# Optimization experiments

Hardware: AMD Instinct MI355X
Metric: run time of the kernel (lower is better)

## Reference

```python
import jax, jax.numpy as jnp
import numpy as np

N_NODES = 100000
N_EDGES = 1000000
D = 64
N_GRAPHS = 128
N_LAYERS = 3
BN_EPS = 1e-5


def setup_inputs() -> dict:
    key = jax.random.key(0)
    ks = jax.random.split(key, 8)
    x = jax.random.normal(ks[0], (N_NODES, D), dtype=jnp.float32)
    edge_index = jax.random.randint(ks[1], (2, N_EDGES), 0, N_NODES, dtype=jnp.int64)
    edge_attr = jax.random.uniform(ks[2], (N_EDGES,), dtype=jnp.float32)
    batch = jnp.sort(jax.random.randint(ks[3], (N_NODES,), 0, N_GRAPHS, dtype=jnp.int64))
    # xavier-uniform linear weights [L, out, in], zero conv bias (PyG GCNConv adds bias after aggregation)
    limit = float(np.sqrt(6.0 / (D + D)))
    W = jax.random.uniform(ks[4], (N_LAYERS, D, D), minval=-limit, maxval=limit, dtype=jnp.float32)
    b = jnp.zeros((N_LAYERS, D), dtype=jnp.float32)
    prelu_a = jnp.asarray(0.25, dtype=jnp.float32)  # single PReLU shared across layers
    bn_w = jnp.ones((N_LAYERS, D), dtype=jnp.float32)
    bn_b = jnp.zeros((N_LAYERS, D), dtype=jnp.float32)
    return {"x": x, "edge_index": edge_index, "edge_attr": edge_attr, "batch": batch,
            "W": W, "b": b, "prelu_a": prelu_a, "bn_w": bn_w, "bn_b": bn_b}


def reference(x, edge_index, edge_attr, batch, W, b, prelu_a, bn_w, bn_b):
    src, dst = edge_index[0], edge_index[1]
    h = x
    pooled = []
    for i in range(N_LAYERS):
        # GCNConv (normalize=False, add_self_loops=False): lin -> weighted scatter-add -> bias
        h = h @ W[i].T                                      # [N, D]
        msg = h[src] * edge_attr[:, None]                   # [E, D] gather + scale
        h = jax.ops.segment_sum(msg, dst, num_segments=N_NODES) + b[i]
        # shared PReLU
        h = jnp.where(h >= 0, h, prelu_a * h)
        # BatchNorm1d (training mode: biased batch stats over nodes)
        mean = jnp.mean(h, axis=0)
        var = jnp.mean((h - mean) ** 2, axis=0)
        h = (h - mean) * jax.lax.rsqrt(var + BN_EPS) * bn_w[i] + bn_b[i]
        pooled.append(jax.ops.segment_sum(h, batch, num_segments=N_GRAPHS))
    global_rep = jnp.concatenate(pooled, axis=1)            # [G, L*D]
    x_stack = pooled[-1]                                    # [G, D]
    return (global_rep, x_stack)
```

## Files before the change

kernel.cpp:

```cpp
#include <hip/hip_runtime.h>

#define NNODES 100000
#define NEDGES 1000000
#define DIM 64
#define NGRAPHS 128
#define NLAYERS 3
#define BN_EPS 1e-5f

#define BINSZ 8
#define NBINS 12500
#define GBLK 256
#define ECHUNK 3907
#define SLICES 4

#define OFF_EDGES   0
#define OFF_BINBASE 2000000
#define OFF_AGG     2012544
#define OFF_YBF     8412544
#define OFF_XBF     11612544
#define OFF_CNT     14812544
#define OFF_OFS     16412544
#define OFF_BTOT    18012544
#define OFF_GSUM4   18025088
#define OFF_PQ4     18057856
#define OFF_SCALE   18090624
#define OFF_SHIFT   18090816
#define OFF_END     18091008

__device__ __forceinline__ unsigned pack_bf16(float a, float b) {
    unsigned ua = __float_as_uint(a), ub = __float_as_uint(b);
    ua = (ua + 0x7FFFu + ((ua >> 16) & 1u)) >> 16;
    ub = (ub + 0x7FFFu + ((ub >> 16) & 1u)) & 0xFFFF0000u;
    return ua | ub;
}

__global__ __launch_bounds__(1024) void count_kernel(const int* __restrict__ ei,
                                                     const float* __restrict__ x,
                                                     const int* __restrict__ batch,
                                                     unsigned short* __restrict__ counts,
                                                     unsigned* __restrict__ xbf,
                                                     int* __restrict__ endv) {
    __shared__ int hist[NBINS];
    const int tid = threadIdx.x, blk = blockIdx.x;
    for (int i = tid; i < NBINS; i += 1024) hist[i] = 0;
    __syncthreads();
    const int e0 = blk * ECHUNK, e1 = min(NEDGES, e0 + ECHUNK);
    for (int e = e0 + tid; e < e1; e += 1024)
        atomicAdd(&hist[ei[NEDGES + e] >> 3], 1);
    __syncthreads();
    unsigned short* crow = counts + (size_t)blk * NBINS;
    for (int bin = tid; bin < NBINS; bin += 1024)
        crow[bin] = (unsigned short)hist[bin];
    const int gtid = blk * 1024 + tid;
    for (int i = gtid; i < NNODES * 32; i += GBLK * 1024) {
        const float2 v = *(const float2*)(x + (size_t)i * 2);
        xbf[i] = pack_bf16(v.x, v.y);
    }
    for (int i = gtid; i < NNODES; i += GBLK * 1024) {
        const int b0 = batch[i];
        const int b1 = (i + 1 < NNODES) ? batch[i + 1] : NGRAPHS;
        for (int g = b0; g < b1; ++g) endv[g] = i + 1;
        if (i == 0)
            for (int g = 0; g < b0; ++g) endv[g] = 0;
    }
}

__global__ __launch_bounds__(256) void s1_kernel(const unsigned short* __restrict__ counts,
                                                 unsigned short* __restrict__ offs,
                                                 int* __restrict__ btot) {
    const int bin = blockIdx.x * 256 + threadIdx.x;
    if (bin >= NBINS) return;
    int run = 0;
    for (int blk = 0; blk < GBLK; ++blk) {
        const int v = counts[(size_t)blk * NBINS + bin];
        offs[(size_t)blk * NBINS + bin] = (unsigned short)run;
        run += v;
    }
    btot[bin] = run;
}

__global__ __launch_bounds__(1024) void s2_kernel(const int* __restrict__ btot,
                                                  int* __restrict__ binBase) {
    __shared__ int wsum[16];
    const int t = threadIdx.x, wid = t >> 6, lane = t & 63;
    int running = 0;
    for (int b = 0; b < NBINS; b += 1024) {
        const int i = b + t;
        const int v = (i < NBINS) ? btot[i] : 0;
        int s = v;
        for (int off = 1; off < 64; off <<= 1) {
            int x = __shfl_up(s, off);
            if (lane >= off) s += x;
        }
        __syncthreads();
        if (lane == 63) wsum[wid] = s;
        __syncthreads();
        int pw = 0, tot = 0;
#pragma unroll
        for (int k = 0; k < 16; ++k) {
            const int x = wsum[k];
            tot += x;
            if (k < wid) pw += x;
        }
        if (i < NBINS) binBase[i] = running + pw + s - v;
        running += tot;
    }
    if (t == 0) binBase[NBINS] = running;
}

__global__ __launch_bounds__(1024) void scatter_kernel(const int* __restrict__ ei,
                                                       const float* __restrict__ ea,
                                                       const int* __restrict__ binBase,
                                                       const unsigned short* __restrict__ offs,
                                                       int2* __restrict__ edges) {
    __shared__ int cur[NBINS];
    const int tid = threadIdx.x, blk = blockIdx.x;
    const unsigned short* orow = offs + (size_t)blk * NBINS;
    for (int i = tid; i < NBINS; i += 1024)
        cur[i] = binBase[i] + (int)orow[i];
    __syncthreads();
    const int e0 = blk * ECHUNK, e1 = min(NEDGES, e0 + ECHUNK);
    for (int e = e0 + tid; e < e1; e += 1024) {
        const int dst = ei[NEDGES + e];
        const int src = ei[e];
        const float w = ea[e];
        const int pos = atomicAdd(&cur[dst >> 3], 1);
        edges[pos] = make_int2((src << 3) | (dst & (BINSZ - 1)), __float_as_int(w));
    }
}

template <bool FIRST>
__global__ __launch_bounds__(256) void agg_kernel(const unsigned* __restrict__ hbf,
                                                  const float* __restrict__ scale,
                                                  const float* __restrict__ shift,
                                                  const int* __restrict__ binBase,
                                                  const int2* __restrict__ edges,
                                                  float* __restrict__ agg) {
    __shared__ float accAll[4][2][BINSZ * 64];
    const int w = threadIdx.x >> 6, lane = threadIdx.x & 63;
    const int bin = blockIdx.x * 4 + w;
    const int half = lane >> 5, p = lane & 31, c0 = 2 * p;
    float* ac = accAll[w][half];
#pragma unroll
    for (int r = 0; r < BINSZ; ++r) *(float2*)&ac[r * 64 + c0] = make_float2(0.f, 0.f);
    float sc0 = 1.f, sc1 = 1.f, sh0 = 0.f, sh1 = 0.f;
    if (!FIRST) { sc0 = scale[c0]; sc1 = scale[c0 + 1]; sh0 = shift[c0]; sh1 = shift[c0 + 1]; }
    const int beg = binBase[bin], end = binBase[bin + 1];
    for (int j = beg; j < end; j += 64) {
        const int n = min(64, end - j);
        int2 ed = (j + lane < end) ? edges[j + lane] : make_int2(0, 0);
        const int n16 = n & ~15;
        int t = 0;
        for (; t < n16; t += 16) {
            int sd_[8]; float wt_[8]; unsigned u_[8];
#pragma unroll
            for (int q = 0; q < 8; ++q) {
                const int ii = t + 2 * q + half;
                sd_[q] = __shfl(ed.x, ii);
                wt_[q] = __int_as_float(__shfl(ed.y, ii));
            }
#pragma unroll
            for (int q = 0; q < 8; ++q) u_[q] = hbf[(size_t)(sd_[q] >> 3) * 32 + p];
#pragma unroll
            for (int q = 0; q < 8; ++q) {
                float h0 = __uint_as_float(u_[q] << 16);
                float h1 = __uint_as_float(u_[q] & 0xFFFF0000u);
                if (!FIRST) { h0 = fmaf(h0, sc0, sh0); h1 = fmaf(h1, sc1, sh1); }
                float2* a2 = (float2*)&ac[(sd_[q] & 7) * 64 + c0];
                float2 v = *a2;
                v.x = fmaf(wt_[q], h0, v.x);
                v.y = fmaf(wt_[q], h1, v.y);
                *a2 = v;
            }
        }
        for (; t < n; t += 2) {
            const int ii = min(t + half, n - 1);
            const int sd = __shfl(ed.x, ii);
            float wt = __int_as_float(__shfl(ed.y, ii));
            if (t + half >= n) wt = 0.f;
            const unsigned u = hbf[(size_t)(sd >> 3) * 32 + p];
            float h0 = __uint_as_float(u << 16);
            float h1 = __uint_as_float(u & 0xFFFF0000u);
            if (!FIRST) { h0 = fmaf(h0, sc0, sh0); h1 = fmaf(h1, sc1, sh1); }
            float2* a2 = (float2*)&ac[(sd & 7) * 64 + c0];
            float2 v = *a2;
            v.x = fmaf(wt, h0, v.x);
            v.y = fmaf(wt, h1, v.y);
            *a2 = v;
        }
    }
    const int nodeBase = bin * BINSZ;
#pragma unroll
    for (int r = 0; r < BINSZ; ++r)
        agg[(size_t)(nodeBase + r) * 64 + lane] =
            accAll[w][0][r * 64 + lane] + accAll[w][1][r * 64 + lane];
}

__global__ __launch_bounds__(256) void gemm_kernel(const float* __restrict__ agg,
                                                   const float* __restrict__ W,
                                                   const float* __restrict__ bias,
                                                   const float* __restrict__ pa_ptr,
                                                   unsigned* __restrict__ ybf) {
    __shared__ float As[128 * 68];
    __shared__ float Wt[64 * 68];
    const int tid = threadIdx.x;
    const int base = blockIdx.x * 128;
    for (int i = tid; i < 2048; i += 256) {
        const int r = i >> 4;
        const int q = (i & 15) * 4;
        const int row = base + r;
        float4 v = make_float4(0.f, 0.f, 0.f, 0.f);
        if (row < NNODES) v = *(const float4*)(agg + (size_t)row * 64 + q);
        *(float4*)&As[r * 68 + q] = v;
    }
    for (int i = tid; i < 4096; i += 256)
        Wt[(i & 63) * 68 + (i >> 6)] = W[i];
    __syncthreads();

    const int tc = tid & 7;
    const int tr = tid >> 3;
    float acc[4][8];
#pragma unroll
    for (int j = 0; j < 4; ++j)
#pragma unroll
        for (int c = 0; c < 8; ++c) acc[j][c] = 0.f;

    for (int kc = 0; kc < 16; ++kc) {
        const int k0 = kc * 4;
        float Af[4][4];
#pragma unroll
        for (int j = 0; j < 4; ++j) {
            const float4 t = *(const float4*)&As[(tr + 32 * j) * 68 + k0];
            Af[j][0] = t.x; Af[j][1] = t.y; Af[j][2] = t.z; Af[j][3] = t.w;
        }
#pragma unroll
        for (int kk = 0; kk < 4; ++kk) {
            const float4 w0 = *(const float4*)&Wt[(k0 + kk) * 68 + tc * 8];
            const float4 w1 = *(const float4*)&Wt[(k0 + kk) * 68 + tc * 8 + 4];
#pragma unroll
            for (int j = 0; j < 4; ++j) {
                const float a = Af[j][kk];
                acc[j][0] = fmaf(a, w0.x, acc[j][0]);
                acc[j][1] = fmaf(a, w0.y, acc[j][1]);
                acc[j][2] = fmaf(a, w0.z, acc[j][2]);
                acc[j][3] = fmaf(a, w0.w, acc[j][3]);
                acc[j][4] = fmaf(a, w1.x, acc[j][4]);
                acc[j][5] = fmaf(a, w1.y, acc[j][5]);
                acc[j][6] = fmaf(a, w1.z, acc[j][6]);
                acc[j][7] = fmaf(a, w1.w, acc[j][7]);
            }
        }
    }

    const float pa = *pa_ptr;
    const float4 b0 = *(const float4*)(bias + tc * 8);
    const float4 b1 = *(const float4*)(bias + tc * 8 + 4);
#pragma unroll
    for (int j = 0; j < 4; ++j) {
        const int row = base + tr + 32 * j;
        if (row >= NNODES) continue;
        float o[8];
        o[0] = acc[j][0] + b0.x; o[1] = acc[j][1] + b0.y;
        o[2] = acc[j][2] + b0.z; o[3] = acc[j][3] + b0.w;
        o[4] = acc[j][4] + b1.x; o[5] = acc[j][5] + b1.y;
        o[6] = acc[j][6] + b1.z; o[7] = acc[j][7] + b1.w;
#pragma unroll
        for (int c = 0; c < 8; ++c) o[c] = (o[c] >= 0.f) ? o[c] : pa * o[c];
        uint4 pk;
        pk.x = pack_bf16(o[0], o[1]);
        pk.y = pack_bf16(o[2], o[3]);
        pk.z = pack_bf16(o[4], o[5]);
        pk.w = pack_bf16(o[6], o[7]);
        *(uint4*)(ybf + (size_t)row * 32 + tc * 4) = pk;
    }
}

__global__ __launch_bounds__(256) void stats_kernel(const unsigned* __restrict__ ybf,
                                                    const int* __restrict__ endv,
                                                    float* __restrict__ gsum4,
                                                    float* __restrict__ pQ4) {
    __shared__ float red[2][32][66];
    const int g = blockIdx.x >> 2, s = blockIdx.x & 3;
    const int t = threadIdx.x, rg = t >> 3, cg = t & 7;
    const int g0 = (g == 0) ? 0 : endv[g - 1];
    const int g1 = endv[g];
    const int len = g1 - g0;
    const int q0 = g0 + (len * s) / SLICES;
    const int q1 = g0 + (len * (s + 1)) / SLICES;
    float sm[8], sq[8];
#pragma unroll
    for (int k = 0; k < 8; ++k) { sm[k] = 0.f; sq[k] = 0.f; }
    for (int r = q0 + rg; r < q1; r += 32) {
        const uint4 u4 = *(const uint4*)&ybf[(size_t)r * 32 + cg * 4];
        const unsigned uu[4] = {u4.x, u4.y, u4.z, u4.w};
#pragma unroll
        for (int k = 0; k < 4; ++k) {
            const float f0 = __uint_as_float(uu[k] << 16);
            const float f1 = __uint_as_float(uu[k] & 0xFFFF0000u);
            sm[2 * k] += f0; sm[2 * k + 1] += f1;
            sq[2 * k] = fmaf(f0, f0, sq[2 * k]);
            sq[2 * k + 1] = fmaf(f1, f1, sq[2 * k + 1]);
        }
    }
#pragma unroll
    for (int k = 0; k < 8; ++k) {
        red[0][rg][cg * 8 + k] = sm[k];
        red[1][rg][cg * 8 + k] = sq[k];
    }
    __syncthreads();
    if (t < 128) {
        const int which = t >> 6, c = t & 63;
        float a = 0.f;
#pragma unroll
        for (int k = 0; k < 32; ++k) a += red[which][k][c];
        if (which == 0) gsum4[blockIdx.x * 64 + c] = a;
        else            pQ4[blockIdx.x * 64 + c] = a;
    }
}

__global__ __launch_bounds__(512) void finalize_kernel(const float* __restrict__ gsum4,
                                                       const float* __restrict__ pQ4,
                                                       const int* __restrict__ endv,
                                                       const float* __restrict__ bn_w,
                                                       const float* __restrict__ bn_b,
                                                       float* __restrict__ scale,
                                                       float* __restrict__ shift,
                                                       float* __restrict__ out, int layer) {
    __shared__ float rS[8][64], rQ[8][64];
    __shared__ float ssc[64], ssh[64];
    const int tid = threadIdx.x;
    const int c = tid & 63, pp = tid >> 6;
    float S = 0.f, Q = 0.f;
    for (int sl = pp; sl < NGRAPHS * SLICES; sl += 8) {
        S += gsum4[sl * 64 + c];
        Q += pQ4[sl * 64 + c];
    }
    rS[pp][c] = S; rQ[pp][c] = Q;
    __syncthreads();
    if (tid < 64) {
        float SS = 0.f, QQ = 0.f;
#pragma unroll
        for (int k = 0; k < 8; ++k) { SS += rS[k][c]; QQ += rQ[k][c]; }
        const float mean = SS * (1.f / NNODES);
        const float var = fmaxf(QQ * (1.f / NNODES) - mean * mean, 0.f);
        const float inv = rsqrtf(var + BN_EPS);
        const float scv = inv * bn_w[c];
        const float shv = bn_b[c] - mean * scv;
        ssc[c] = scv; ssh[c] = shv;
        scale[c] = scv; shift[c] = shv;
    }
    __syncthreads();
    for (int idx = tid; idx < NGRAPHS * 64; idx += 512) {
        const int g = idx >> 6, ch = idx & 63;
        float gs = 0.f;
#pragma unroll
        for (int sl = 0; sl < SLICES; ++sl) gs += gsum4[(g * SLICES + sl) * 64 + ch];
        const int cnt = endv[g] - ((g == 0) ? 0 : endv[g - 1]);
        const float pooled = gs * ssc[ch] + (float)cnt * ssh[ch];
        out[g * (NLAYERS * 64) + layer * 64 + ch] = pooled;
        if (layer == NLAYERS - 1) out[NGRAPHS * NLAYERS * 64 + idx] = pooled;
    }
}

extern "C" void kernel_launch(void* const* d_in, const int* in_sizes, int n_in,
                              void* d_out, int out_size, void* d_ws, size_t ws_size,
                              hipStream_t stream) {
    const float* x     = (const float*)d_in[0];
    const int*   ei    = (const int*)d_in[1];
    const float* ea    = (const float*)d_in[2];
    const int*   batch = (const int*)d_in[3];
    const float* W     = (const float*)d_in[4];
    const float* b     = (const float*)d_in[5];
    const float* pa    = (const float*)d_in[6];
    const float* bn_w  = (const float*)d_in[7];
    const float* bn_b  = (const float*)d_in[8];
    float* out = (float*)d_out;
    float* ws  = (float*)d_ws;
    int*   wsi = (int*)d_ws;

    int2*           edges   = (int2*)(wsi + OFF_EDGES);
    int*            binBase = wsi + OFF_BINBASE;
    float*          agg     = ws + OFF_AGG;
    unsigned*       ybf     = (unsigned*)(wsi + OFF_YBF);
    unsigned*       xbf     = (unsigned*)(wsi + OFF_XBF);
    unsigned short* counts  = (unsigned short*)(wsi + OFF_CNT);
    unsigned short* offs    = (unsigned short*)(wsi + OFF_OFS);
    int*            btot    = wsi + OFF_BTOT;
    float*          gsum4   = ws + OFF_GSUM4;
    float*          pQ4     = ws + OFF_PQ4;
    float*          scaleA  = ws + OFF_SCALE;
    float*          shiftA  = ws + OFF_SHIFT;
    int*            endv    = wsi + OFF_END;

    count_kernel<<<GBLK, 1024, 0, stream>>>(ei, x, batch, counts, xbf, endv);
    s1_kernel<<<(NBINS + 255) / 256, 256, 0, stream>>>(counts, offs, btot);
    s2_kernel<<<1, 1024, 0, stream>>>(btot, binBase);
    scatter_kernel<<<GBLK, 1024, 0, stream>>>(ei, ea, binBase, offs, edges);

    for (int l = 0; l < NLAYERS; ++l) {
        if (l == 0)
            agg_kernel<true><<<NBINS / 4, 256, 0, stream>>>(xbf, nullptr, nullptr,
                                                            binBase, edges, agg);
        else
            agg_kernel<false><<<NBINS / 4, 256, 0, stream>>>(ybf, scaleA + (l - 1) * 64,
                                                             shiftA + (l - 1) * 64,
                                                             binBase, edges, agg);
        gemm_kernel<<<(NNODES + 127) / 128, 256, 0, stream>>>(agg, W + l * 4096, b + l * 64,
                                                              pa, ybf);
        stats_kernel<<<NGRAPHS * SLICES, 256, 0, stream>>>(ybf, endv, gsum4, pQ4);
        finalize_kernel<<<1, 512, 0, stream>>>(gsum4, pQ4, endv, bn_w + l * 64,
                                               bn_b + l * 64, scaleA + l * 64,
                                               shiftA + l * 64, out, l);
    }
}
```

Measured before the change: 295.3 us.

## Store aggregation output as bf16 and fuse BN finalize into stats via last-block counter

The aggregation kernel now writes its per-node sums as packed bf16 instead of fp32, and the GEMM unpacks them. This halves the traffic of the agg intermediate. Separately, the stats and finalize kernels are merged: the last block to finish, found through an atomic counter with threadfences, computes the BN scale and shift and the pooled outputs, which removes one launch per layer. The cost is an extra bf16 rounding of the aggregated values before the GEMM, and the counters must be reset, which count_kernel does.

```diff
diff --git a/kernel.cpp b/kernel.cpp
--- a/kernel.cpp
+++ b/kernel.cpp
@@ -12,6 +12,7 @@
 #define GBLK 256
 #define ECHUNK 3907
 #define SLICES 4
+#define SBLK (NGRAPHS * SLICES)
 
 #define OFF_EDGES   0
 #define OFF_BINBASE 2000000
@@ -26,6 +27,7 @@
 #define OFF_SCALE   18090624
 #define OFF_SHIFT   18090816
 #define OFF_END     18091008
+#define OFF_CTR     18091136
 
 __device__ __forceinline__ unsigned pack_bf16(float a, float b) {
     unsigned ua = __float_as_uint(a), ub = __float_as_uint(b);
@@ -33,13 +35,16 @@
     ub = (ub + 0x7FFFu + ((ub >> 16) & 1u)) & 0xFFFF0000u;
     return ua | ub;
 }
+__device__ __forceinline__ float bflo(unsigned u) { return __uint_as_float(u << 16); }
+__device__ __forceinline__ float bfhi(unsigned u) { return __uint_as_float(u & 0xFFFF0000u); }
 
 __global__ __launch_bounds__(1024) void count_kernel(const int* __restrict__ ei,
                                                      const float* __restrict__ x,
                                                      const int* __restrict__ batch,
                                                      unsigned short* __restrict__ counts,
                                                      unsigned* __restrict__ xbf,
-                                                     int* __restrict__ endv) {
+                                                     int* __restrict__ endv,
+                                                     int* __restrict__ ctr) {
     __shared__ int hist[NBINS];
     const int tid = threadIdx.x, blk = blockIdx.x;
     for (int i = tid; i < NBINS; i += 1024) hist[i] = 0;
@@ -63,6 +68,7 @@
         if (i == 0)
             for (int g = 0; g < b0; ++g) endv[g] = 0;
     }
+    if (gtid < NLAYERS) ctr[gtid] = 0;
 }
 
 __global__ __launch_bounds__(256) void s1_kernel(const unsigned short* __restrict__ counts,
@@ -135,7 +141,7 @@
                                                   const float* __restrict__ shift,
                                                   const int* __restrict__ binBase,
                                                   const int2* __restrict__ edges,
-                                                  float* __restrict__ agg) {
+                                                  unsigned* __restrict__ aggbf) {
     __shared__ float accAll[4][2][BINSZ * 64];
     const int w = threadIdx.x >> 6, lane = threadIdx.x & 63;
     const int bin = blockIdx.x * 4 + w;
@@ -163,8 +169,8 @@
             for (int q = 0; q < 8; ++q) u_[q] = hbf[(size_t)(sd_[q] >> 3) * 32 + p];
 #pragma unroll
             for (int q = 0; q < 8; ++q) {
-                float h0 = __uint_as_float(u_[q] << 16);
-                float h1 = __uint_as_float(u_[q] & 0xFFFF0000u);
+                float h0 = bflo(u_[q]);
+                float h1 = bfhi(u_[q]);
                 if (!FIRST) { h0 = fmaf(h0, sc0, sh0); h1 = fmaf(h1, sc1, sh1); }
                 float2* a2 = (float2*)&ac[(sd_[q] & 7) * 64 + c0];
                 float2 v = *a2;
@@ -179,8 +185,8 @@
             float wt = __int_as_float(__shfl(ed.y, ii));
             if (t + half >= n) wt = 0.f;
             const unsigned u = hbf[(size_t)(sd >> 3) * 32 + p];
-            float h0 = __uint_as_float(u << 16);
-            float h1 = __uint_as_float(u & 0xFFFF0000u);
+            float h0 = bflo(u);
+            float h1 = bfhi(u);
             if (!FIRST) { h0 = fmaf(h0, sc0, sh0); h1 = fmaf(h1, sc1, sh1); }
             float2* a2 = (float2*)&ac[(sd & 7) * 64 + c0];
             float2 v = *a2;
@@ -191,12 +197,16 @@
     }
     const int nodeBase = bin * BINSZ;
 #pragma unroll
-    for (int r = 0; r < BINSZ; ++r)
-        agg[(size_t)(nodeBase + r) * 64 + lane] =
-            accAll[w][0][r * 64 + lane] + accAll[w][1][r * 64 + lane];
-}
-
-__global__ __launch_bounds__(256) void gemm_kernel(const float* __restrict__ agg,
+    for (int i = 0; i < 4; ++i) {
+        const int idx = lane + 64 * i;
+        const int r = idx >> 5, p2 = idx & 31;
+        const float2 a0 = *(const float2*)&accAll[w][0][r * 64 + 2 * p2];
+        const float2 a1 = *(const float2*)&accAll[w][1][r * 64 + 2 * p2];
+        aggbf[(size_t)(nodeBase + r) * 32 + p2] = pack_bf16(a0.x + a1.x, a0.y + a1.y);
+    }
+}
+
+__global__ __launch_bounds__(256) void gemm_kernel(const unsigned* __restrict__ aggbf,
                                                    const float* __restrict__ W,
                                                    const float* __restrict__ bias,
                                                    const float* __restrict__ pa_ptr,
@@ -207,11 +217,14 @@
     const int base = blockIdx.x * 128;
     for (int i = tid; i < 2048; i += 256) {
         const int r = i >> 4;
-        const int q = (i & 15) * 4;
+        const int q = i & 15;
         const int row = base + r;
         float4 v = make_float4(0.f, 0.f, 0.f, 0.f);
-        if (row < NNODES) v = *(const float4*)(agg + (size_t)row * 64 + q);
-        *(float4*)&As[r * 68 + q] = v;
+        if (row < NNODES) {
+            const uint2 u = *(const uint2*)&aggbf[(size_t)row * 32 + q * 2];
+            v = make_float4(bflo(u.x), bfhi(u.x), bflo(u.y), bfhi(u.y));
+        }
+        *(float4*)&As[r * 68 + q * 4] = v;
     }
     for (int i = tid; i < 4096; i += 256)
         Wt[(i & 63) * 68 + (i >> 6)] = W[i];
@@ -275,13 +288,20 @@
     }
 }
 
-__global__ __launch_bounds__(256) void stats_kernel(const unsigned* __restrict__ ybf,
-                                                    const int* __restrict__ endv,
-                                                    float* __restrict__ gsum4,
-                                                    float* __restrict__ pQ4) {
+__global__ __launch_bounds__(256) void statsfin_kernel(const unsigned* __restrict__ ybf,
+                                                       const int* __restrict__ endv,
+                                                       float* __restrict__ gsum4,
+                                                       float* __restrict__ pQ4,
+                                                       const float* __restrict__ bn_w,
+                                                       const float* __restrict__ bn_b,
+                                                       float* __restrict__ scale,
+                                                       float* __restrict__ shift,
+                                                       float* __restrict__ out, int layer,
+                                                       int* __restrict__ ctr) {
     __shared__ float red[2][32][66];
+    __shared__ int amLast;
     const int g = blockIdx.x >> 2, s = blockIdx.x & 3;
-    const int t = threadIdx.x, rg = t >> 3, cg = t & 7;
+    const int tid = threadIdx.x, rg = tid >> 3, cg = tid & 7;
     const int g0 = (g == 0) ? 0 : endv[g - 1];
     const int g1 = endv[g];
     const int len = g1 - g0;
@@ -295,8 +315,8 @@
         const unsigned uu[4] = {u4.x, u4.y, u4.z, u4.w};
 #pragma unroll
         for (int k = 0; k < 4; ++k) {
-            const float f0 = __uint_as_float(uu[k] << 16);
-            const float f1 = __uint_as_float(uu[k] & 0xFFFF0000u);
+            const float f0 = bflo(uu[k]);
+            const float f1 = bfhi(uu[k]);
             sm[2 * k] += f0; sm[2 * k + 1] += f1;
             sq[2 * k] = fmaf(f0, f0, sq[2 * k]);
             sq[2 * k + 1] = fmaf(f1, f1, sq[2 * k + 1]);
@@ -308,30 +328,27 @@
         red[1][rg][cg * 8 + k] = sq[k];
     }
     __syncthreads();
-    if (t < 128) {
-        const int which = t >> 6, c = t & 63;
+    if (tid < 128) {
+        const int which = tid >> 6, c = tid & 63;
         float a = 0.f;
 #pragma unroll
         for (int k = 0; k < 32; ++k) a += red[which][k][c];
         if (which == 0) gsum4[blockIdx.x * 64 + c] = a;
         else            pQ4[blockIdx.x * 64 + c] = a;
     }
-}
-
-__global__ __launch_bounds__(512) void finalize_kernel(const float* __restrict__ gsum4,
-                                                       const float* __restrict__ pQ4,
-                                                       const int* __restrict__ endv,
-                                                       const float* __restrict__ bn_w,
-                                                       const float* __restrict__ bn_b,
-                                                       float* __restrict__ scale,
-                                                       float* __restrict__ shift,
-                                                       float* __restrict__ out, int layer) {
-    __shared__ float rS[8][64], rQ[8][64];
+    __syncthreads();
+    if (tid == 0) {
+        __threadfence();
+        amLast = (atomicAdd(ctr, 1) == SBLK - 1);
+    }
+    __syncthreads();
+    if (!amLast) return;
+    __threadfence();
+    __shared__ float rS[4][64], rQ[4][64];
     __shared__ float ssc[64], ssh[64];
-    const int tid = threadIdx.x;
     const int c = tid & 63, pp = tid >> 6;
     float S = 0.f, Q = 0.f;
-    for (int sl = pp; sl < NGRAPHS * SLICES; sl += 8) {
+    for (int sl = pp; sl < SBLK; sl += 4) {
         S += gsum4[sl * 64 + c];
         Q += pQ4[sl * 64 + c];
     }
@@ -340,7 +357,7 @@
     if (tid < 64) {
         float SS = 0.f, QQ = 0.f;
 #pragma unroll
-        for (int k = 0; k < 8; ++k) { SS += rS[k][c]; QQ += rQ[k][c]; }
+        for (int k = 0; k < 4; ++k) { SS += rS[k][c]; QQ += rQ[k][c]; }
         const float mean = SS * (1.f / NNODES);
         const float var = fmaxf(QQ * (1.f / NNODES) - mean * mean, 0.f);
         const float inv = rsqrtf(var + BN_EPS);
@@ -350,14 +367,14 @@
         scale[c] = scv; shift[c] = shv;
     }
     __syncthreads();
-    for (int idx = tid; idx < NGRAPHS * 64; idx += 512) {
-        const int g = idx >> 6, ch = idx & 63;
+    for (int idx = tid; idx < NGRAPHS * 64; idx += 256) {
+        const int gg = idx >> 6, ch = idx & 63;
         float gs = 0.f;
 #pragma unroll
-        for (int sl = 0; sl < SLICES; ++sl) gs += gsum4[(g * SLICES + sl) * 64 + ch];
-        const int cnt = endv[g] - ((g == 0) ? 0 : endv[g - 1]);
+        for (int sl = 0; sl < SLICES; ++sl) gs += gsum4[(gg * SLICES + sl) * 64 + ch];
+        const int cnt = endv[gg] - ((gg == 0) ? 0 : endv[gg - 1]);
         const float pooled = gs * ssc[ch] + (float)cnt * ssh[ch];
-        out[g * (NLAYERS * 64) + layer * 64 + ch] = pooled;
+        out[gg * (NLAYERS * 64) + layer * 64 + ch] = pooled;
         if (layer == NLAYERS - 1) out[NGRAPHS * NLAYERS * 64 + idx] = pooled;
     }
 }
@@ -380,7 +397,7 @@
 
     int2*           edges   = (int2*)(wsi + OFF_EDGES);
     int*            binBase = wsi + OFF_BINBASE;
-    float*          agg     = ws + OFF_AGG;
+    unsigned*       aggbf   = (unsigned*)(wsi + OFF_AGG);
     unsigned*       ybf     = (unsigned*)(wsi + OFF_YBF);
     unsigned*       xbf     = (unsigned*)(wsi + OFF_XBF);
     unsigned short* counts  = (unsigned short*)(wsi + OFF_CNT);
@@ -391,8 +408,9 @@
     float*          scaleA  = ws + OFF_SCALE;
     float*          shiftA  = ws + OFF_SHIFT;
     int*            endv    = wsi + OFF_END;
-
-    count_kernel<<<GBLK, 1024, 0, stream>>>(ei, x, batch, counts, xbf, endv);
+    int*            ctr     = wsi + OFF_CTR;
+
+    count_kernel<<<GBLK, 1024, 0, stream>>>(ei, x, batch, counts, xbf, endv, ctr);
     s1_kernel<<<(NBINS + 255) / 256, 256, 0, stream>>>(counts, offs, btot);
     s2_kernel<<<1, 1024, 0, stream>>>(btot, binBase);
     scatter_kernel<<<GBLK, 1024, 0, stream>>>(ei, ea, binBase, offs, edges);
@@ -400,16 +418,16 @@
     for (int l = 0; l < NLAYERS; ++l) {
         if (l == 0)
             agg_kernel<true><<<NBINS / 4, 256, 0, stream>>>(xbf, nullptr, nullptr,
-                                                            binBase, edges, agg);
+                                                            binBase, edges, aggbf);
         else
             agg_kernel<false><<<NBINS / 4, 256, 0, stream>>>(ybf, scaleA + (l - 1) * 64,
                                                              shiftA + (l - 1) * 64,
-                                                             binBase, edges, agg);
-        gemm_kernel<<<(NNODES + 127) / 128, 256, 0, stream>>>(agg, W + l * 4096, b + l * 64,
-                                                              pa, ybf);
-        stats_kernel<<<NGRAPHS * SLICES, 256, 0, stream>>>(ybf, endv, gsum4, pQ4);
-        finalize_kernel<<<1, 512, 0, stream>>>(gsum4, pQ4, endv, bn_w + l * 64,
-                                               bn_b + l * 64, scaleA + l * 64,
-                                               shiftA + l * 64, out, l);
-    }
-}
+                                                             binBase, edges, aggbf);
+        gemm_kernel<<<(NNODES + 127) / 128, 256, 0, stream>>>(aggbf, W + l * 4096,
+                                                              b + l * 64, pa, ybf);
+        statsfin_kernel<<<SBLK, 256, 0, stream>>>(ybf, endv, gsum4, pQ4,
+                                                  bn_w + l * 64, bn_b + l * 64,
+                                                  scaleA + l * 64, shiftA + l * 64,
+                                                  out, l, ctr + l);
+    }
+}
```

Result: slower. 383.1 us (+29.7%).
